# Kernel optimization log

Measured on AMD Instinct MI355X. Metric: run time of the kernel, lower is better.

## Reference

```python
import jax, jax.numpy as jnp
import numpy as np

N_NODES = 100000
N_EDGES = 1600000
EMB_DIM = 128
BN_EPS = 1e-5


def setup_inputs() -> dict:
    key = jax.random.key(0)
    k = jax.random.split(key, 5)
    x = jax.random.normal(k[0], (N_NODES, EMB_DIM), dtype=jnp.float32)
    src = jax.random.randint(k[1], (N_EDGES,), 0, N_NODES)
    dst = jax.random.randint(k[2], (N_EDGES,), 0, N_NODES)
    W = jax.random.normal(k[3], (EMB_DIM, EMB_DIM), dtype=jnp.float32) / np.float32(np.sqrt(EMB_DIM))
    b = jnp.zeros((EMB_DIM,), dtype=jnp.float32)
    gamma = jnp.ones((EMB_DIM,), dtype=jnp.float32)
    beta = jnp.zeros((EMB_DIM,), dtype=jnp.float32)
    return {"x": x, "src": src, "dst": dst, "W": W, "b": b, "gamma": gamma, "beta": beta}


def reference(x, src, dst, W, b, gamma, beta):
    n = x.shape[0]
    ones = jnp.ones(src.shape, dtype=x.dtype)
    # DGL GraphConv norm='both': degrees clamped to min 1
    deg_out = jnp.maximum(jax.ops.segment_sum(ones, src, num_segments=n), 1.0)
    deg_in = jnp.maximum(jax.ops.segment_sum(ones, dst, num_segments=n), 1.0)
    norm_src = jax.lax.rsqrt(deg_out)  # [N]
    norm_dst = jax.lax.rsqrt(deg_in)   # [N]
    # W applied before aggregation (in_feats == out_feats path in DGL)
    h = (x * norm_src[:, None]) @ W                              # [N, D]
    agg = jax.ops.segment_sum(h[src], dst, num_segments=n)       # SpMM gather/scatter, [N, D]
    h = agg * norm_dst[:, None] + b                              # [N, D]
    # BatchNorm1d over nodes (training-mode batch stats, biased variance)
    mean = jnp.mean(h, axis=0)
    var = jnp.var(h, axis=0)
    h = (h - mean) * jax.lax.rsqrt(var + BN_EPS) * gamma + beta
    h = jax.nn.relu(h)
    # dropout: identity in eval-mode reference
    return h + x  # residual
```

## Files before the change

### kernel.cpp

```cpp
#include <hip/hip_runtime.h>
#include <hip/hip_bf16.h>

#define NN 100000
#define NE 1600000
#define D  128
#define BN_EPS 1e-5f

#define CB  782
#define NC  256
#define EPC (NE / NC)
#define NSLICE  4
#define SLICESZ 30800
#define SW      (SLICESZ / 2)
#define SCH     64
#define EPH (NE / SCH)

typedef __attribute__((ext_vector_type(8))) short bf16x8;
typedef __attribute__((ext_vector_type(4))) float f32x4;

#define WLD 136

static __device__ __forceinline__ ushort f2bf(float f) {
    __hip_bfloat16 b = __float2bfloat16(f);
    return *reinterpret_cast<ushort*>(&b);
}
static __device__ __forceinline__ float bflo(unsigned v) {
    return __uint_as_float((v & 0xffffu) << 16);
}
static __device__ __forceinline__ float bfhi(unsigned v) {
    return __uint_as_float(v & 0xffff0000u);
}

__global__ __launch_bounds__(256) void k_front(const int* __restrict__ src,
                                               const int* __restrict__ dst,
                                               const float* __restrict__ W,
                                               ushort* __restrict__ WT,
                                               int* __restrict__ SP,
                                               int* __restrict__ P,
                                               float* __restrict__ stats) {
    __shared__ int hist[SW];
    __shared__ int dh[CB];
    const int t = threadIdx.x;
    const int s = blockIdx.x >> 6;
    const int c = blockIdx.x & 63;
    for (int i = t; i < SW; i += 256) hist[i] = 0;
    for (int i = t; i < CB; i += 256) dh[i] = 0;
    __syncthreads();

    const int lo = s * SLICESZ;
    const int sbase = c * EPH;
    for (int i = t; i < EPH; i += 256) {
        int k = src[sbase + i] - lo;
        if ((unsigned)k < (unsigned)SLICESZ)
            atomicAdd(&hist[k >> 1], 1 << ((k & 1) * 16));
    }
    const int dbase = blockIdx.x * EPC;
    for (int i = t; i < EPC; i += 256)
        atomicAdd(&dh[dst[dbase + i] >> 7], 1);
    __syncthreads();

    int* outS = SP + ((size_t)s * SCH + c) * SW;
    for (int i = t; i < SW; i += 256) outS[i] = hist[i];
    for (int i = t; i < CB; i += 256) P[i * NC + blockIdx.x] = dh[i];

    if (blockIdx.x < 64) {
        int i = blockIdx.x * 256 + t;
        int n = i >> 7, k2 = i & 127;
        WT[i] = f2bf(W[k2 * D + n]);
    }
    if (blockIdx.x == 64) stats[t] = 0.0f;
}


__global__ __launch_bounds__(256) void k_cscanA(int* __restrict__ P,
                                                int* __restrict__ bintotal) {
    __shared__ int sh[NC];
    const int b = blockIdx.x;
    const int t = threadIdx.x;
    const int v = P[b * NC + t];
    sh[t] = v;
    __syncthreads();
    for (int off = 1; off < NC; off <<= 1) {
        int u = (t >= off) ? sh[t - off] : 0;
        __syncthreads();
        sh[t] += u;
        __syncthreads();
    }
    P[b * NC + t] = sh[t] - v;
    if (t == NC - 1) bintotal[b] = sh[t];
}

__global__ __launch_bounds__(1024) void k_cscanB(const int* __restrict__ bintotal,
                                                 int* __restrict__ binbase) {
    __shared__ int sh[1024];
    const int t = threadIdx.x;
    const int v = (t < CB) ? bintotal[t] : 0;
    sh[t] = v;
    __syncthreads();
    for (int off = 1; off < 1024; off <<= 1) {
        int u = (t >= off) ? sh[t - off] : 0;
        __syncthreads();
        sh[t] += u;
        __syncthreads();
    }
    if (t < CB) binbase[t] = sh[t] - v;
    if (t == CB - 1) binbase[CB] = sh[t];
}

__global__ __launch_bounds__(256) void k_cscatter(const int* __restrict__ dst,
                                                  const int* __restrict__ src,
                                                  const int* __restrict__ P,
                                                  const int* __restrict__ binbase,
                                                  int* __restrict__ sedge) {
    __shared__ int cur[CB];
    const int c = blockIdx.x;
    const int t = threadIdx.x;
    for (int i = t; i < CB; i += 256) cur[i] = binbase[i] + P[i * NC + c];
    __syncthreads();
    const int base = c * EPC;
    for (int i = t; i < EPC; i += 256) {
        int d = dst[base + i];
        int pos = atomicAdd(&cur[d >> 7], 1);
        sedge[pos] = src[base + i] | ((d & 127) << 17);
    }
}

__global__ __launch_bounds__(256) void k_fine(const int* __restrict__ sedge,
                                              const int* __restrict__ binbase,
                                              int* __restrict__ ptr,
                                              int* __restrict__ esrc) {
    __shared__ int fh[128], fp[128], fcur[128];
    const int b = blockIdx.x;
    const int t = threadIdx.x;
    const int lo = binbase[b], hi = binbase[b + 1];
    if (t < 128) fh[t] = 0;
    __syncthreads();
    for (int i = lo + t; i < hi; i += 256)
        atomicAdd(&fh[(unsigned)sedge[i] >> 17], 1);
    __syncthreads();
    if (t < 128) fp[t] = fh[t];
    __syncthreads();
    for (int off = 1; off < 128; off <<= 1) {
        int u = (t < 128 && t >= off) ? fp[t - off] : 0;
        __syncthreads();
        if (t < 128) fp[t] += u;
        __syncthreads();
    }
    if (t < 128) {
        const int node = b * 128 + t;
        const int ex = fp[t] - fh[t];
        fcur[t] = ex;
        if (node < NN) {
            ptr[node] = lo + ex;
        } else if (node == NN) {
            ptr[NN] = lo + ex;
        }
    }
    __syncthreads();
    for (int i = lo + t; i < hi; i += 256) {
        unsigned v = (unsigned)sedge[i];
        int pos = atomicAdd(&fcur[v >> 17], 1);
        esrc[lo + pos] = v & 0x1FFFF;
    }
}


__global__ void k_smerge(const int* __restrict__ SP, float* __restrict__ degout) {
    int w = blockIdx.x * 256 + threadIdx.x;
    if (w >= (NN + 1) / 2) return;
    const int n = w * 2;
    const int s = n / SLICESZ;
    const int k = n - s * SLICESZ;
    const int* col = SP + ((size_t)s * SCH) * SW + (k >> 1);
    int lo = 0, hi = 0;
#pragma unroll 8
    for (int c = 0; c < SCH; ++c) {
        int v = col[(size_t)c * SW];
        lo += v & 0xFFFF;
        hi += (v >> 16) & 0xFFFF;
    }
    degout[n] = (float)lo;
    if (n + 1 < NN) degout[n + 1] = (float)hi;
}

__global__ __launch_bounds__(256) void k_gemm(const float* __restrict__ x,
                                              const float* __restrict__ degout,
                                              const ushort* __restrict__ WT,
                                              ushort* __restrict__ h) {
    __shared__ ushort Wl[D * WLD];

    const int t = threadIdx.x;
    for (int s = t; s < 2048; s += 256) {
        int row = s >> 4, slot = s & 15;
        uint4 v = *reinterpret_cast<const uint4*>(WT + row * D + slot * 8);
        *reinterpret_cast<uint4*>(&Wl[row * WLD + slot * 8]) = v;
    }
    __syncthreads();

    const int wave = t >> 6;
    const int lane = t & 63;
    const int m16  = lane & 15;
    const int kq   = lane >> 4;
    const int row  = blockIdx.x * 64 + wave * 16 + m16;
    const int rc   = row < NN ? row : NN - 1;

    const float nrm = rsqrtf(fmaxf(degout[rc], 1.0f));

    bf16x8 afrag[4];
    const float* xr = x + (size_t)rc * D + kq * 8;
#pragma unroll
    for (int kt = 0; kt < 4; ++kt) {
        f32x4 lo = *reinterpret_cast<const f32x4*>(xr + kt * 32);
        f32x4 hi = *reinterpret_cast<const f32x4*>(xr + kt * 32 + 4);
        union { bf16x8 v; ushort u[8]; } af;
#pragma unroll
        for (int j = 0; j < 4; ++j) {
            af.u[j]     = f2bf(lo[j] * nrm);
            af.u[4 + j] = f2bf(hi[j] * nrm);
        }
        afrag[kt] = af.v;
    }

    f32x4 acc[8];
#pragma unroll
    for (int nt = 0; nt < 8; ++nt) acc[nt] = (f32x4)(0.0f);

#pragma unroll
    for (int kt = 0; kt < 4; ++kt) {
#pragma unroll
        for (int nt = 0; nt < 8; ++nt) {
            int n = nt * 16 + m16;
            const bf16x8 bfrag = *reinterpret_cast<const bf16x8*>(
                &Wl[n * WLD + kt * 32 + kq * 8]);
            acc[nt] = __builtin_amdgcn_mfma_f32_16x16x32_bf16(afrag[kt], bfrag, acc[nt], 0, 0, 0);
        }
    }

    const int orow = blockIdx.x * 64 + wave * 16 + kq * 4;
#pragma unroll
    for (int nt = 0; nt < 8; ++nt) {
#pragma unroll
        for (int r = 0; r < 4; ++r) {
            int rr = orow + r;
            if (rr < NN) h[(size_t)rr * D + nt * 16 + m16] = f2bf(acc[nt][r]);
        }
    }
}

__global__ __launch_bounds__(256) void k_agg(const ushort* __restrict__ h,
                                             const int* __restrict__ ptr,
                                             const int* __restrict__ esrc,
                                             const float* __restrict__ b,
                                             ushort* __restrict__ h2) {
    const int node = blockIdx.x * 4 + (threadIdx.x >> 6);
    const int lane = threadIdx.x & 63;
    if (node >= NN) return;
    const int s0 = ptr[node];
    const int s1 = ptr[node + 1];
    const int eg = lane >> 4;
    const int cb = (lane & 15) * 8;

    float acc[8];
#pragma unroll
    for (int j = 0; j < 8; ++j) acc[j] = 0.0f;

    for (int i = s0; i < s1; i += 16) {
        int  idx[4];
        bool p[4];
        uint4 v[4];
#pragma unroll
        for (int u = 0; u < 4; ++u) {
            int ii = i + eg + 4 * u;
            p[u] = ii < s1;
            if (p[u]) idx[u] = esrc[ii];
        }
#pragma unroll
        for (int u = 0; u < 4; ++u)
            if (p[u]) v[u] = *reinterpret_cast<const uint4*>(h + (size_t)idx[u] * D + cb);
#pragma unroll
        for (int u = 0; u < 4; ++u) {
            if (p[u]) {
                acc[0] += bflo(v[u].x); acc[1] += bfhi(v[u].x);
                acc[2] += bflo(v[u].y); acc[3] += bfhi(v[u].y);
                acc[4] += bflo(v[u].z); acc[5] += bfhi(v[u].z);
                acc[6] += bflo(v[u].w); acc[7] += bfhi(v[u].w);
            }
        }
    }
#pragma unroll
    for (int j = 0; j < 8; ++j) {
        acc[j] += __shfl_xor(acc[j], 16, 64);
        acc[j] += __shfl_xor(acc[j], 32, 64);
    }
    if (eg == 0) {
        const float nrm = rsqrtf(fmaxf((float)(s1 - s0), 1.0f));
        uint4 o;
        unsigned w[4];
#pragma unroll
        for (int m = 0; m < 4; ++m) {
            float e0 = acc[2 * m]     * nrm + b[cb + 2 * m];
            float e1 = acc[2 * m + 1] * nrm + b[cb + 2 * m + 1];
            w[m] = (unsigned)f2bf(e0) | ((unsigned)f2bf(e1) << 16);
        }
        o.x = w[0]; o.y = w[1]; o.z = w[2]; o.w = w[3];
        *reinterpret_cast<uint4*>(h2 + (size_t)node * D + cb) = o;
    }
}

__global__ __launch_bounds__(256) void k_stats(const unsigned* __restrict__ h2u,
                                               float* __restrict__ stats) {
    __shared__ float red[4][256];
    const int t = threadIdx.x;
    float s1lo = 0.f, s1hi = 0.f, s2lo = 0.f, s2hi = 0.f;
    const int total = NN * (D / 2);
    const int stride = gridDim.x * 256;
    for (int i = blockIdx.x * 256 + t; i < total; i += stride) {
        unsigned v = h2u[i];
        float lo = bflo(v), hi = bfhi(v);
        s1lo += lo; s1hi += hi;
        s2lo += lo * lo; s2hi += hi * hi;
    }
    red[0][t] = s1lo; red[1][t] = s1hi; red[2][t] = s2lo; red[3][t] = s2hi;
    __syncthreads();
    if (t < 64) {
        const int c = t * 2;
        float a0 = red[0][t] + red[0][t + 64] + red[0][t + 128] + red[0][t + 192];
        float a1 = red[1][t] + red[1][t + 64] + red[1][t + 128] + red[1][t + 192];
        float q0 = red[2][t] + red[2][t + 64] + red[2][t + 128] + red[2][t + 192];
        float q1 = red[3][t] + red[3][t + 64] + red[3][t + 128] + red[3][t + 192];
        atomicAdd(&stats[c], a0);
        atomicAdd(&stats[c + 1], a1);
        atomicAdd(&stats[128 + c], q0);
        atomicAdd(&stats[128 + c + 1], q1);
    }
}

__global__ void k_final(const uint2* __restrict__ h2v, const float4* __restrict__ xv,
                        const float* __restrict__ gamma, const float* __restrict__ beta,
                        const float* __restrict__ stats, float4* __restrict__ outv) {
    const int i = blockIdx.x * 256 + threadIdx.x;
    const int total = NN * (D / 4);
    if (i >= total) return;
    const int c = (i & 31) * 4;
    const float inv_n = 1.0f / (float)NN;
    uint2 v = h2v[i];
    float4 xx = xv[i];
    float hv[4] = { bflo(v.x), bfhi(v.x), bflo(v.y), bfhi(v.y) };
    float xr[4] = { xx.x, xx.y, xx.z, xx.w };
    float o[4];
#pragma unroll
    for (int m = 0; m < 4; ++m) {
        float mean = stats[c + m] * inv_n;
        float var  = stats[128 + c + m] * inv_n - mean * mean;
        float t = (hv[m] - mean) * rsqrtf(var + BN_EPS) * gamma[c + m] + beta[c + m];
        o[m] = fmaxf(t, 0.0f) + xr[m];
    }
    float4 ov; ov.x = o[0]; ov.y = o[1]; ov.z = o[2]; ov.w = o[3];
    outv[i] = ov;
}

extern "C" void kernel_launch(void* const* d_in, const int* in_sizes, int n_in,
                              void* d_out, int out_size, void* d_ws, size_t ws_size,
                              hipStream_t stream) {
    const float* x     = (const float*)d_in[0];
    const int*   src   = (const int*)d_in[1];
    const int*   dst   = (const int*)d_in[2];
    const float* W     = (const float*)d_in[3];
    const float* b     = (const float*)d_in[4];
    const float* gamma = (const float*)d_in[5];
    const float* beta  = (const float*)d_in[6];
    float* out = (float*)d_out;

    float* ws     = (float*)d_ws;
    ushort* h2    = (ushort*)ws;
    float* degout = ws + (size_t)NN * D;
    float* stats  = degout + NN;
    int*   ptr    = (int*)(stats + 256);
    int*   esrc   = ptr + (NN + 1);
    ushort* WT    = (ushort*)(esrc + NE);

    int* sedge    = (int*)ws;
    int* SP       = sedge + NE;
    int* P        = SP + (size_t)NSLICE * SCH * SW;
    int* bintotal = P + (size_t)CB * NC;
    int* binbase  = bintotal + CB;

    ushort* h = (ushort*)d_out;

    k_front<<<NSLICE * SCH, 256, 0, stream>>>(src, dst, W, WT, SP, P, stats);
    k_cscanA<<<CB, 256, 0, stream>>>(P, bintotal);
    k_cscanB<<<1, 1024, 0, stream>>>(bintotal, binbase);
    k_cscatter<<<NC, 256, 0, stream>>>(dst, src, P, binbase, sedge);
    k_smerge<<<((NN + 1) / 2 + 255) / 256, 256, 0, stream>>>(SP, degout);
    k_gemm<<<(NN + 63) / 64, 256, 0, stream>>>(x, degout, WT, h);
    k_fine<<<CB, 256, 0, stream>>>(sedge, binbase, ptr, esrc);
    k_agg<<<(NN + 3) / 4, 256, 0, stream>>>(h, ptr, esrc, b, h2);
    k_stats<<<1024, 256, 0, stream>>>((const unsigned*)h2, stats);
    k_final<<<(NN * (D / 4) + 255) / 256, 256, 0, stream>>>((const uint2*)h2, (const float4*)x,
                                                            gamma, beta, stats, (float4*)out);
}
```

Before: 244.7 us.

## Pack out-degree histogram as 8-bit counters over 2 slices and 256 chunks

The out-degree histogram now packs four 8-bit counters per LDS word, so two node slices cover the graph instead of four. Src indices are now re-read twice instead of four times. The edge range is split into 256 chunks, and only slice-0 blocks build the dst bin histogram. The merge kernel unpacks four bytes per word and sums over 256 partial histograms. This raises the partial-histogram storage written and re-read several-fold, and silently overflows if any node has more than 255 out-edges within one chunk.

```diff
diff --git a/kernel.cpp b/kernel.cpp
--- a/kernel.cpp
+++ b/kernel.cpp
@@ -9,10 +9,10 @@
 #define CB  782
 #define NC  256
 #define EPC (NE / NC)
-#define NSLICE  4
-#define SLICESZ 30800
-#define SW      (SLICESZ / 2)
-#define SCH     64
+#define NSLICE  2
+#define SLICESZ 61600
+#define SW      (SLICESZ / 4)
+#define SCH     256
 #define EPH (NE / SCH)
 
 typedef __attribute__((ext_vector_type(8))) short bf16x8;
@@ -41,34 +41,35 @@
     __shared__ int hist[SW];
     __shared__ int dh[CB];
     const int t = threadIdx.x;
-    const int s = blockIdx.x >> 6;
-    const int c = blockIdx.x & 63;
+    const int s = blockIdx.x >> 8;
+    const int c = blockIdx.x & 255;
     for (int i = t; i < SW; i += 256) hist[i] = 0;
     for (int i = t; i < CB; i += 256) dh[i] = 0;
     __syncthreads();
 
     const int lo = s * SLICESZ;
-    const int sbase = c * EPH;
+    const int base = c * EPH;
     for (int i = t; i < EPH; i += 256) {
-        int k = src[sbase + i] - lo;
+        int k = src[base + i] - lo;
         if ((unsigned)k < (unsigned)SLICESZ)
-            atomicAdd(&hist[k >> 1], 1 << ((k & 1) * 16));
-    }
-    const int dbase = blockIdx.x * EPC;
-    for (int i = t; i < EPC; i += 256)
-        atomicAdd(&dh[dst[dbase + i] >> 7], 1);
-    __syncthreads();
-
-    int* outS = SP + ((size_t)s * SCH + c) * SW;
+            atomicAdd(&hist[k >> 2], 1 << ((k & 3) * 8));
+    }
+    if (s == 0) {
+        for (int i = t; i < EPH; i += 256)
+            atomicAdd(&dh[dst[base + i] >> 7], 1);
+    }
+    __syncthreads();
+
+    int* outS = SP + (size_t)blockIdx.x * SW;
     for (int i = t; i < SW; i += 256) outS[i] = hist[i];
-    for (int i = t; i < CB; i += 256) P[i * NC + blockIdx.x] = dh[i];
-
-    if (blockIdx.x < 64) {
-        int i = blockIdx.x * 256 + t;
+    if (s == 0)
+        for (int i = t; i < CB; i += 256) P[i * NC + c] = dh[i];
+    if (s == 1 && c < 64) {
+        int i = c * 256 + t;
         int n = i >> 7, k2 = i & 127;
         WT[i] = f2bf(W[k2 * D + n]);
     }
-    if (blockIdx.x == 64) stats[t] = 0.0f;
+    if (s == 1 && c == 64) stats[t] = 0.0f;
 }
 
 
@@ -167,20 +168,24 @@
 
 __global__ void k_smerge(const int* __restrict__ SP, float* __restrict__ degout) {
     int w = blockIdx.x * 256 + threadIdx.x;
-    if (w >= (NN + 1) / 2) return;
-    const int n = w * 2;
-    const int s = n / SLICESZ;
-    const int k = n - s * SLICESZ;
-    const int* col = SP + ((size_t)s * SCH) * SW + (k >> 1);
-    int lo = 0, hi = 0;
+    if (w >= NSLICE * SW) return;
+    const int s = w / SW, wi = w - s * SW;
+    const int n0 = s * SLICESZ + wi * 4;
+    if (n0 >= NN) return;
+    const int* col = SP + (size_t)s * SCH * SW + wi;
+    int b0 = 0, b1 = 0, b2 = 0, b3 = 0;
 #pragma unroll 8
     for (int c = 0; c < SCH; ++c) {
-        int v = col[(size_t)c * SW];
-        lo += v & 0xFFFF;
-        hi += (v >> 16) & 0xFFFF;
-    }
-    degout[n] = (float)lo;
-    if (n + 1 < NN) degout[n + 1] = (float)hi;
+        unsigned v = (unsigned)col[(size_t)c * SW];
+        b0 += v & 0xFF;
+        b1 += (v >> 8) & 0xFF;
+        b2 += (v >> 16) & 0xFF;
+        b3 += (v >> 24);
+    }
+    degout[n0] = (float)b0;
+    if (n0 + 1 < NN) degout[n0 + 1] = (float)b1;
+    if (n0 + 2 < NN) degout[n0 + 2] = (float)b2;
+    if (n0 + 3 < NN) degout[n0 + 3] = (float)b3;
 }
 
 __global__ __launch_bounds__(256) void k_gemm(const float* __restrict__ x,
@@ -391,7 +396,7 @@
     k_cscanA<<<CB, 256, 0, stream>>>(P, bintotal);
     k_cscanB<<<1, 1024, 0, stream>>>(bintotal, binbase);
     k_cscatter<<<NC, 256, 0, stream>>>(dst, src, P, binbase, sedge);
-    k_smerge<<<((NN + 1) / 2 + 255) / 256, 256, 0, stream>>>(SP, degout);
+    k_smerge<<<(NSLICE * SW + 255) / 256, 256, 0, stream>>>(SP, degout);
     k_gemm<<<(NN + 63) / 64, 256, 0, stream>>>(x, degout, WT, h);
     k_fine<<<CB, 256, 0, stream>>>(sedge, binbase, ptr, esrc);
     k_agg<<<(NN + 3) / 4, 256, 0, stream>>>(h, ptr, esrc, b, h2);
```

After: 231.8 us. -5.3%, faster.
